# Kernel tuning notes

Measured on AMD Instinct MI355X. Metric: run time of the kernel, lower is better.

## Reference

```python
import jax, jax.numpy as jnp
import numpy as np

N = 65536
IN_DIM = 512
H1, H2 = 256, 128
LATENT = 3
SINDY_DIM = 22  # latent=3, poly_order=3: 3 ones + 3 linear + 6 quad + 10 cubic


def _mlp(v, w0, b0, w1, b1, w2, b2):
    # Linear+Sigmoid, Linear+Sigmoid, Linear+Identity (matches encoder/decoder stacks)
    h = jax.nn.sigmoid(v @ w0 + b0)
    h = jax.nn.sigmoid(h @ w1 + b1)
    return h @ w2 + b2


def _sindy_library(z):
    # Faithful to sindy_library(): d ones columns, then linear, quad (i<=j), cubic (i<=j<=k)
    n, d = z.shape
    cols = [jnp.ones((n,), z.dtype) for _ in range(d)]
    cols += [z[:, i] for i in range(d)]
    for i in range(d):
        for j in range(i, d):
            cols.append(z[:, i] * z[:, j])
    for i in range(d):
        for j in range(i, d):
            for k in range(j, d):
                cols.append(z[:, i] * z[:, j] * z[:, k])
    return jnp.stack(cols, axis=1)


def _mean_jac(fn, x):
    # torch: jacobian of batched fn, take block-diagonal (per-sample Jacobians), mean over samples
    return jax.vmap(jax.jacrev(fn))(x).mean(axis=0)


def setup_inputs():
    key = jax.random.key(0)
    ks = jax.random.split(key, 12)

    def glorot(k, i, o):
        return jax.random.normal(k, (i, o), jnp.float32) * np.float32(np.sqrt(2.0 / (i + o)))

    return {
        "x": jax.random.normal(ks[0], (N, IN_DIM), jnp.float32),
        "dx": jax.random.normal(ks[1], (N, IN_DIM), jnp.float32),
        "ddx": jax.random.normal(ks[2], (N, IN_DIM), jnp.float32),
        "enc_w0": glorot(ks[3], IN_DIM, H1), "enc_b0": jnp.zeros((H1,), jnp.float32),
        "enc_w1": glorot(ks[4], H1, H2), "enc_b1": jnp.zeros((H2,), jnp.float32),
        "enc_w2": glorot(ks[5], H2, LATENT), "enc_b2": jnp.zeros((LATENT,), jnp.float32),
        "dec_w0": glorot(ks[6], LATENT, H2), "dec_b0": jnp.zeros((H2,), jnp.float32),
        "dec_w1": glorot(ks[7], H2, H1), "dec_b1": jnp.zeros((H1,), jnp.float32),
        "dec_w2": glorot(ks[8], H1, IN_DIM), "dec_b2": jnp.zeros((IN_DIM,), jnp.float32),
        "E_w": jnp.ones((SINDY_DIM, LATENT), jnp.float32),  # nn.init.ones_ on E.weight
        "E_b": jnp.zeros((LATENT,), jnp.float32),
    }


def reference(x, dx, ddx, enc_w0, enc_b0, enc_w1, enc_b1, enc_w2, enc_b2,
              dec_w0, dec_b0, dec_w1, dec_b1, dec_w2, dec_b2, E_w, E_b):
    enc = lambda v: _mlp(v, enc_w0, enc_b0, enc_w1, enc_b1, enc_w2, enc_b2)
    dec = lambda v: _mlp(v, dec_w0, dec_b0, dec_w1, dec_b1, dec_w2, dec_b2)

    z = enc(x)                      # [N, LATENT]
    Je = _mean_jac(enc, x)          # [LATENT, IN_DIM]  batch-mean encoder Jacobian
    dz = dx @ Je.T                  # [N, LATENT]
    theta = _sindy_library(z)       # [N, SINDY_DIM]
    dzb = theta @ E_w + E_b         # [N, LATENT]  SINDy prediction E(theta)
    xb = dec(z)                     # [N, IN_DIM]
    Jd = _mean_jac(dec, z)          # [IN_DIM, LATENT]  batch-mean decoder Jacobian
    dxb = dzb @ Jd.T                # [N, IN_DIM]
    return (z, dz, dzb, xb, dxb)
```

## Files before the change

### kernel.cpp

```cpp
#include <hip/hip_runtime.h>

#define NROWS 65536

typedef unsigned short u16;
typedef short bf16x8 __attribute__((ext_vector_type(8)));
typedef u16 u16x8 __attribute__((ext_vector_type(8)));
typedef float f32x4 __attribute__((ext_vector_type(4)));

__device__ __forceinline__ u16 f2bf(float f) {
  unsigned int u = __builtin_bit_cast(unsigned int, f);
  u += 0x7FFFu + ((u >> 16) & 1u);
  return (u16)(u >> 16);
}
__device__ __forceinline__ float bf2f(u16 s) {
  return __builtin_bit_cast(float, (unsigned int)s << 16);
}

__global__ void prep_weights(const float* __restrict__ eW0, const float* __restrict__ eW1,
                             const float* __restrict__ dW1, const float* __restrict__ dW2,
                             u16* __restrict__ eW0t, u16* __restrict__ eW1t,
                             u16* __restrict__ dW1t, u16* __restrict__ dW2t) {
  const int idx = blockIdx.x * 256 + threadIdx.x;
  if (idx < 131072) {
    const int n = idx >> 9, k = idx & 511;
    eW0t[idx] = f2bf(eW0[k * 256 + n]);
  } else if (idx < 163840) {
    const int j = idx - 131072, n = j >> 8, k = j & 255;
    eW1t[j] = f2bf(eW1[k * 128 + n]);
  } else if (idx < 196608) {
    const int j = idx - 163840, n = j >> 7, k = j & 127;
    dW1t[j] = f2bf(dW1[k * 256 + n]);
  } else {
    const int j = idx - 196608, n = j >> 8, k = j & 255;
    dW2t[j] = f2bf(dW2[k * 512 + n]);
  }
}

template <int ACT, int A_F32>
__global__ __launch_bounds__(256, 2) void gemm_mfma(const void* __restrict__ Av,
                                                    const u16* __restrict__ Wt,
                                                    const float* __restrict__ bias,
                                                    void* __restrict__ Cv, int K, int Nc) {
  __shared__ u16 As[128 * 32];
  __shared__ u16 Bs[128 * 32];
  const int tid = threadIdx.x;
  const int lane = tid & 63;
  const int wave = tid >> 6;
  const int n0 = blockIdx.x * 128;
  const int m0 = blockIdx.y * 128;
  const int wm = (wave & 1) * 64;
  const int wn = (wave >> 1) * 64;
  const int q = lane >> 4;
  const int mr = lane & 15;

  f32x4 acc[4][4] = {};

  for (int k0 = 0; k0 < K; k0 += 32) {
    if (A_F32) {
      const float* A = (const float*)Av;
#pragma unroll
      for (int i = 0; i < 2; ++i) {
        const int c = tid + i * 256;
        const int r = c >> 2, p = c & 3;
        const int g = (p - (r >> 1)) & 3;
        const float* src = A + (size_t)(m0 + r) * K + k0 + g * 8;
        const float4 v0 = *(const float4*)src;
        const float4 v1 = *(const float4*)(src + 4);
        u16x8 w;
        w[0] = f2bf(v0.x); w[1] = f2bf(v0.y); w[2] = f2bf(v0.z); w[3] = f2bf(v0.w);
        w[4] = f2bf(v1.x); w[5] = f2bf(v1.y); w[6] = f2bf(v1.z); w[7] = f2bf(v1.w);
        *(u16x8*)&As[c * 8] = w;
      }
    } else {
      const u16* A = (const u16*)Av;
#pragma unroll
      for (int i = 0; i < 2; ++i) {
        const int c = tid + i * 256;
        const int r = c >> 2, p = c & 3;
        const int g = (p - (r >> 1)) & 3;
        __builtin_amdgcn_global_load_lds(
            (const __attribute__((address_space(1))) void*)(A + (size_t)(m0 + r) * K + k0 + g * 8),
            (__attribute__((address_space(3))) void*)&As[(i * 256 + wave * 64) * 8], 16, 0, 0);
      }
    }
    {
#pragma unroll
      for (int i = 0; i < 2; ++i) {
        const int c = tid + i * 256;
        const int r = c >> 2, p = c & 3;
        const int g = (p - (r >> 1)) & 3;
        __builtin_amdgcn_global_load_lds(
            (const __attribute__((address_space(1))) void*)(Wt + (size_t)(n0 + r) * K + k0 + g * 8),
            (__attribute__((address_space(3))) void*)&Bs[(i * 256 + wave * 64) * 8], 16, 0, 0);
      }
    }
    __syncthreads();

    bf16x8 af[4], bfr[4];
#pragma unroll
    for (int i = 0; i < 4; ++i) {
      const int r = wm + i * 16 + mr;
      const int col = (q + (r >> 1)) & 3;
      af[i] = *(const bf16x8*)&As[r * 32 + col * 8];
    }
#pragma unroll
    for (int j = 0; j < 4; ++j) {
      const int r = wn + j * 16 + mr;
      const int col = (q + (r >> 1)) & 3;
      bfr[j] = *(const bf16x8*)&Bs[r * 32 + col * 8];
    }
#pragma unroll
    for (int i = 0; i < 4; ++i)
#pragma unroll
      for (int j = 0; j < 4; ++j)
        acc[i][j] = __builtin_amdgcn_mfma_f32_16x16x32_bf16(af[i], bfr[j], acc[i][j], 0, 0, 0);
    __syncthreads();
  }

  const int orow = (lane >> 4) * 4;
  const int ocol = lane & 15;
#pragma unroll
  for (int j = 0; j < 4; ++j) {
    const int col = n0 + wn + j * 16 + ocol;
    const float bj = bias[col];
#pragma unroll
    for (int i = 0; i < 4; ++i) {
      const int rbase = m0 + wm + i * 16 + orow;
#pragma unroll
      for (int r = 0; r < 4; ++r) {
        float v = acc[i][j][r] + bj;
        if (ACT) {
          v = 1.0f / (1.0f + __expf(-v));
          ((u16*)Cv)[(size_t)(rbase + r) * Nc + col] = f2bf(v);
        } else {
          ((float*)Cv)[(size_t)(rbase + r) * Nc + col] = v;
        }
      }
    }
  }
}

__global__ void covar_bf16(const u16* __restrict__ P, const u16* __restrict__ Q,
                           float* __restrict__ partial, int Ap, int Bq, int chunk) {
  __shared__ float Ps[16][68];
  __shared__ float Qs[16][68];
  const int tid = threadIdx.x;
  const int a0 = blockIdx.x * 64;
  const int b0 = blockIdx.y * 64;
  const int nbase = blockIdx.z * chunk;
  const int tx = tid & 15, ty = tid >> 4;
  float acc[4][4] = {};
  for (int nn = 0; nn < chunk; nn += 16) {
    const int e = tid * 4;
    const int r = e >> 6;
    const int c = e & 63;
    {
      const ushort4 v = *(const ushort4*)(P + (size_t)(nbase + nn + r) * Ap + (a0 + c));
      const float p0 = bf2f(v.x), p1 = bf2f(v.y), p2 = bf2f(v.z), p3 = bf2f(v.w);
      Ps[r][c + 0] = p0 * (1.0f - p0);
      Ps[r][c + 1] = p1 * (1.0f - p1);
      Ps[r][c + 2] = p2 * (1.0f - p2);
      Ps[r][c + 3] = p3 * (1.0f - p3);
    }
    {
      const ushort4 u = *(const ushort4*)(Q + (size_t)(nbase + nn + r) * Bq + (b0 + c));
      const float q0 = bf2f(u.x), q1 = bf2f(u.y), q2 = bf2f(u.z), q3 = bf2f(u.w);
      Qs[r][c + 0] = q0 * (1.0f - q0);
      Qs[r][c + 1] = q1 * (1.0f - q1);
      Qs[r][c + 2] = q2 * (1.0f - q2);
      Qs[r][c + 3] = q3 * (1.0f - q3);
    }
    __syncthreads();
#pragma unroll
    for (int kk = 0; kk < 16; ++kk) {
      float a[4], b[4];
#pragma unroll
      for (int i = 0; i < 4; ++i) a[i] = Ps[kk][ty * 4 + i];
#pragma unroll
      for (int j = 0; j < 4; ++j) b[j] = Qs[kk][tx * 4 + j];
#pragma unroll
      for (int i = 0; i < 4; ++i)
#pragma unroll
        for (int j = 0; j < 4; ++j) acc[i][j] += a[i] * b[j];
    }
    __syncthreads();
  }
  float* out = partial + (size_t)blockIdx.z * Ap * Bq;
#pragma unroll
  for (int i = 0; i < 4; ++i)
#pragma unroll
    for (int j = 0; j < 4; ++j)
      out[(size_t)(a0 + ty * 4 + i) * Bq + (b0 + tx * 4 + j)] = acc[i][j];
}

__global__ void reduce_partial(const float* __restrict__ partial, float* __restrict__ out,
                               int S, int Z) {
  const int i = blockIdx.x * 256 + threadIdx.x;
  float s = 0.f;
  for (int z = 0; z < Z; ++z) s += partial[(size_t)z * S + i];
  out[i] = s;
}

__global__ void enc_l3_sindy(const u16* __restrict__ h2, const float* __restrict__ W2,
                             const float* __restrict__ b2, const float* __restrict__ Ew,
                             const float* __restrict__ Eb, float* __restrict__ z_out,
                             float* __restrict__ dzb_out) {
  const int lane = threadIdx.x & 63;
  const int row = blockIdx.x * 4 + (threadIdx.x >> 6);
  const ushort2 h = *(const ushort2*)(h2 + (size_t)row * 128 + lane * 2);
  const float hx = bf2f(h.x), hy = bf2f(h.y);
  const int k = lane * 2;
  float s[3];
#pragma unroll
  for (int l = 0; l < 3; ++l)
    s[l] = hx * W2[k * 3 + l] + hy * W2[(k + 1) * 3 + l];
#pragma unroll
  for (int off = 32; off > 0; off >>= 1) {
    s[0] += __shfl_xor(s[0], off);
    s[1] += __shfl_xor(s[1], off);
    s[2] += __shfl_xor(s[2], off);
  }
  if (lane == 0) {
    const float z0 = s[0] + b2[0];
    const float z1 = s[1] + b2[1];
    const float z2 = s[2] + b2[2];
    z_out[row * 3 + 0] = z0;
    z_out[row * 3 + 1] = z1;
    z_out[row * 3 + 2] = z2;
    float th[22];
    th[0] = 1.f; th[1] = 1.f; th[2] = 1.f;
    th[3] = z0; th[4] = z1; th[5] = z2;
    th[6] = z0 * z0; th[7] = z0 * z1; th[8] = z0 * z2;
    th[9] = z1 * z1; th[10] = z1 * z2; th[11] = z2 * z2;
    th[12] = z0 * z0 * z0; th[13] = z0 * z0 * z1; th[14] = z0 * z0 * z2;
    th[15] = z0 * z1 * z1; th[16] = z0 * z1 * z2; th[17] = z0 * z2 * z2;
    th[18] = z1 * z1 * z1; th[19] = z1 * z1 * z2; th[20] = z1 * z2 * z2;
    th[21] = z2 * z2 * z2;
    float d0 = Eb[0], d1 = Eb[1], d2 = Eb[2];
#pragma unroll
    for (int c = 0; c < 22; ++c) {
      d0 += th[c] * Ew[c * 3 + 0];
      d1 += th[c] * Ew[c * 3 + 1];
      d2 += th[c] * Ew[c * 3 + 2];
    }
    dzb_out[row * 3 + 0] = d0;
    dzb_out[row * 3 + 1] = d1;
    dzb_out[row * 3 + 2] = d2;
  }
}

__global__ void t1_kernel(const float* __restrict__ Ce, const float* __restrict__ W2,
                          const float* __restrict__ W1, float* __restrict__ T1) {
  const int l = blockIdx.x;
  const int b = threadIdx.x;
  float acc = 0.f;
  for (int a = 0; a < 128; ++a)
    acc += W2[a * 3 + l] * W1[b * 128 + a] * Ce[a * 256 + b];
  T1[l * 256 + b] = acc * (1.0f / 65536.0f);
}

__global__ void je_kernel(const float* __restrict__ T1, const float* __restrict__ W0,
                          float* __restrict__ Je) {
  const int k = blockIdx.x * 256 + threadIdx.x;
  const int l = blockIdx.y;
  float acc = 0.f;
  for (int b = 0; b < 256; ++b) acc += T1[l * 256 + b] * W0[(size_t)k * 256 + b];
  Je[l * 512 + k] = acc;
}

__global__ void t2_kernel(const float* __restrict__ Cd, const float* __restrict__ V1,
                          const float* __restrict__ V0, float* __restrict__ T2) {
  const int l = blockIdx.x;
  const int a = threadIdx.x;
  float acc = 0.f;
  for (int b = 0; b < 128; ++b)
    acc += Cd[a * 128 + b] * V1[b * 256 + a] * V0[l * 128 + b];
  T2[a * 3 + l] = acc * (1.0f / 65536.0f);
}

__global__ void jd_kernel(const float* __restrict__ T2, const float* __restrict__ V2,
                          float* __restrict__ Jd) {
  const int k = blockIdx.x * 256 + threadIdx.x;
  const int l = blockIdx.y;
  float acc = 0.f;
  for (int a = 0; a < 256; ++a) acc += V2[(size_t)a * 512 + k] * T2[a * 3 + l];
  Jd[k * 3 + l] = acc;
}

__global__ void dz_kernel(const float* __restrict__ dx, const float* __restrict__ Je,
                          float* __restrict__ dz) {
  __shared__ float sJe[1536];
  for (int i = threadIdx.x; i < 1536; i += 256) sJe[i] = Je[i];
  __syncthreads();
  const int lane = threadIdx.x & 63;
  const int row = blockIdx.x * 4 + (threadIdx.x >> 6);
  const int k = lane * 8;
  const float4 v0 = *(const float4*)(dx + (size_t)row * 512 + k);
  const float4 v1 = *(const float4*)(dx + (size_t)row * 512 + k + 4);
  float s[3];
#pragma unroll
  for (int l = 0; l < 3; ++l) {
    const float* j = sJe + l * 512 + k;
    s[l] = v0.x * j[0] + v0.y * j[1] + v0.z * j[2] + v0.w * j[3] +
           v1.x * j[4] + v1.y * j[5] + v1.z * j[6] + v1.w * j[7];
  }
#pragma unroll
  for (int off = 32; off > 0; off >>= 1) {
    s[0] += __shfl_xor(s[0], off);
    s[1] += __shfl_xor(s[1], off);
    s[2] += __shfl_xor(s[2], off);
  }
  if (lane == 0) {
    dz[row * 3 + 0] = s[0];
    dz[row * 3 + 1] = s[1];
    dz[row * 3 + 2] = s[2];
  }
}

__global__ void dec_l1(const float* __restrict__ z, const float* __restrict__ V0,
                       const float* __restrict__ b0, u16* __restrict__ h1d) {
  __shared__ float sW[512];
  for (int i = threadIdx.x; i < 512; i += 256)
    sW[i] = (i < 384) ? V0[i] : b0[i - 384];
  __syncthreads();
  const int idx = blockIdx.x * 256 + threadIdx.x;
  const int n = idx >> 7;
  const int j = idx & 127;
  const float z0 = z[n * 3 + 0], z1 = z[n * 3 + 1], z2 = z[n * 3 + 2];
  const float v = z0 * sW[j] + z1 * sW[128 + j] + z2 * sW[256 + j] + sW[384 + j];
  h1d[idx] = f2bf(1.0f / (1.0f + __expf(-v)));
}

__global__ void dxb_kernel(const float* __restrict__ dzb, const float* __restrict__ Jd,
                           float* __restrict__ dxb) {
  __shared__ float sJd[1536];
  for (int i = threadIdx.x; i < 1536; i += 256) sJd[i] = Jd[i];
  __syncthreads();
  const int idx = blockIdx.x * 256 + threadIdx.x;
  const int n = idx >> 9;
  const int k = idx & 511;
  const float d0 = dzb[n * 3 + 0], d1 = dzb[n * 3 + 1], d2 = dzb[n * 3 + 2];
  dxb[idx] = d0 * sJd[k * 3 + 0] + d1 * sJd[k * 3 + 1] + d2 * sJd[k * 3 + 2];
}

extern "C" void kernel_launch(void* const* d_in, const int* in_sizes, int n_in,
                              void* d_out, int out_size, void* d_ws, size_t ws_size,
                              hipStream_t stream) {
  const int N = NROWS;
  const float* x   = (const float*)d_in[0];
  const float* dx  = (const float*)d_in[1];
  const float* eW0 = (const float*)d_in[3];
  const float* eb0 = (const float*)d_in[4];
  const float* eW1 = (const float*)d_in[5];
  const float* eb1 = (const float*)d_in[6];
  const float* eW2 = (const float*)d_in[7];
  const float* eb2 = (const float*)d_in[8];
  const float* dW0 = (const float*)d_in[9];
  const float* db0 = (const float*)d_in[10];
  const float* dW1 = (const float*)d_in[11];
  const float* db1 = (const float*)d_in[12];
  const float* dW2 = (const float*)d_in[13];
  const float* db2 = (const float*)d_in[14];
  const float* Ew  = (const float*)d_in[15];
  const float* Eb  = (const float*)d_in[16];

  float* out = (float*)d_out;
  float* z_out   = out;
  float* dz_out  = out + (size_t)N * 3;
  float* dzb_out = out + (size_t)N * 6;
  float* xb_out  = out + (size_t)N * 9;
  float* dxb_out = out + (size_t)N * 9 + (size_t)N * 512;

  u16* h1e = (u16*)d_ws;
  u16* h2e = h1e + (size_t)N * 256;
  u16* h2d = h1e;
  u16* h1d = h2e;
  u16* wbuf = h2e + (size_t)N * 128;
  u16* eW0t = wbuf;
  u16* eW1t = eW0t + 131072;
  u16* dW1t = eW1t + 32768;
  u16* dW2t = dW1t + 32768;
  float* partial = (float*)(dW2t + 131072);
  float* Ce = partial + (size_t)128 * 32768;
  float* Cd = Ce + 32768;
  float* T1 = Cd + 32768;
  float* T2 = T1 + 768;
  float* Je = T2 + 768;
  float* Jd = Je + 1536;

  prep_weights<<<1280, 256, 0, stream>>>(eW0, eW1, dW1, dW2, eW0t, eW1t, dW1t, dW2t);

  gemm_mfma<1, 1><<<dim3(2, N / 128), 256, 0, stream>>>(x, eW0t, eb0, h1e, 512, 256);
  gemm_mfma<1, 0><<<dim3(1, N / 128), 256, 0, stream>>>(h1e, eW1t, eb1, h2e, 256, 128);
  enc_l3_sindy<<<N / 4, 256, 0, stream>>>(h2e, eW2, eb2, Ew, Eb, z_out, dzb_out);

  covar_bf16<<<dim3(2, 4, 128), 256, 0, stream>>>(h2e, h1e, partial, 128, 256, N / 128);
  reduce_partial<<<128, 256, 0, stream>>>(partial, Ce, 32768, 128);
  t1_kernel<<<3, 256, 0, stream>>>(Ce, eW2, eW1, T1);
  je_kernel<<<dim3(2, 3), 256, 0, stream>>>(T1, eW0, Je);
  dz_kernel<<<N / 4, 256, 0, stream>>>(dx, Je, dz_out);

  dec_l1<<<N * 128 / 256, 256, 0, stream>>>(z_out, dW0, db0, h1d);
  gemm_mfma<1, 0><<<dim3(2, N / 128), 256, 0, stream>>>(h1d, dW1t, db1, h2d, 128, 256);
  gemm_mfma<0, 0><<<dim3(4, N / 128), 256, 0, stream>>>(h2d, dW2t, db2, xb_out, 256, 512);

  covar_bf16<<<dim3(4, 2, 128), 256, 0, stream>>>(h2d, h1d, partial, 256, 128, N / 128);
  reduce_partial<<<128, 256, 0, stream>>>(partial, Cd, 32768, 128);
  t2_kernel<<<3, 256, 0, stream>>>(Cd, dW1, dW0, T2);
  jd_kernel<<<dim3(2, 3), 256, 0, stream>>>(T2, dW2, Jd);
  dxb_kernel<<<N * 512 / 256, 256, 0, stream>>>(dzb_out, Jd, dxb_out);
}
```

Measured before the change: 965.1 us.

## Enlarge covariance tiles, fuse Jacobian kernels, vectorize decoder-L1 and dxb kernels

The covariance kernel moves to 128x128 tiles with 8x8 register blocking per thread and vectorized LDS and global accesses, so it does more FMA work per shared-memory load. The T1/Je and T2/Jd kernel pairs are each merged into a single 768-thread block that keeps the intermediate in shared memory, removing two launches. dec_l1 and dxb now have each thread produce 8 contiguous outputs with vector stores and keep weights in registers instead of shared memory. In exchange, the covariance kernel runs fewer blocks with higher register pressure, and the fused Jacobian kernels run on a single block.

```diff
diff --git a/kernel.cpp b/kernel.cpp
--- a/kernel.cpp
+++ b/kernel.cpp
@@ -14,6 +14,10 @@
 }
 __device__ __forceinline__ float bf2f(u16 s) {
   return __builtin_bit_cast(float, (unsigned int)s << 16);
+}
+__device__ __forceinline__ float sigd(u16 s) {
+  const float p = bf2f(s);
+  return p * (1.0f - p);
 }
 
 __global__ void prep_weights(const float* __restrict__ eW0, const float* __restrict__ eW1,
@@ -140,57 +144,66 @@
   }
 }
 
-__global__ void covar_bf16(const u16* __restrict__ P, const u16* __restrict__ Q,
-                           float* __restrict__ partial, int Ap, int Bq, int chunk) {
-  __shared__ float Ps[16][68];
-  __shared__ float Qs[16][68];
+__global__ __launch_bounds__(256, 2) void covar128(const u16* __restrict__ P,
+                                                   const u16* __restrict__ Q,
+                                                   float* __restrict__ partial,
+                                                   int Ap, int Bq, int chunk) {
+  __shared__ float Ps[16][132];
+  __shared__ float Qs[16][132];
   const int tid = threadIdx.x;
-  const int a0 = blockIdx.x * 64;
-  const int b0 = blockIdx.y * 64;
+  const int a0 = blockIdx.x * 128;
+  const int b0 = blockIdx.y * 128;
   const int nbase = blockIdx.z * chunk;
   const int tx = tid & 15, ty = tid >> 4;
-  float acc[4][4] = {};
+  float acc[8][8] = {};
+
   for (int nn = 0; nn < chunk; nn += 16) {
-    const int e = tid * 4;
-    const int r = e >> 6;
-    const int c = e & 63;
     {
-      const ushort4 v = *(const ushort4*)(P + (size_t)(nbase + nn + r) * Ap + (a0 + c));
-      const float p0 = bf2f(v.x), p1 = bf2f(v.y), p2 = bf2f(v.z), p3 = bf2f(v.w);
-      Ps[r][c + 0] = p0 * (1.0f - p0);
-      Ps[r][c + 1] = p1 * (1.0f - p1);
-      Ps[r][c + 2] = p2 * (1.0f - p2);
-      Ps[r][c + 3] = p3 * (1.0f - p3);
+      const u16* pr = P + (size_t)(nbase + nn + ty) * Ap + a0;
+      const ushort4 v0 = *(const ushort4*)(pr + tx * 4);
+      const ushort4 v1 = *(const ushort4*)(pr + 64 + tx * 4);
+      float4 f0, f1;
+      f0.x = sigd(v0.x); f0.y = sigd(v0.y); f0.z = sigd(v0.z); f0.w = sigd(v0.w);
+      f1.x = sigd(v1.x); f1.y = sigd(v1.y); f1.z = sigd(v1.z); f1.w = sigd(v1.w);
+      *(float4*)&Ps[ty][tx * 4] = f0;
+      *(float4*)&Ps[ty][64 + tx * 4] = f1;
     }
     {
-      const ushort4 u = *(const ushort4*)(Q + (size_t)(nbase + nn + r) * Bq + (b0 + c));
-      const float q0 = bf2f(u.x), q1 = bf2f(u.y), q2 = bf2f(u.z), q3 = bf2f(u.w);
-      Qs[r][c + 0] = q0 * (1.0f - q0);
-      Qs[r][c + 1] = q1 * (1.0f - q1);
-      Qs[r][c + 2] = q2 * (1.0f - q2);
-      Qs[r][c + 3] = q3 * (1.0f - q3);
+      const u16* qr = Q + (size_t)(nbase + nn + ty) * Bq + b0;
+      const ushort4 v0 = *(const ushort4*)(qr + tx * 4);
+      const ushort4 v1 = *(const ushort4*)(qr + 64 + tx * 4);
+      float4 f0, f1;
+      f0.x = sigd(v0.x); f0.y = sigd(v0.y); f0.z = sigd(v0.z); f0.w = sigd(v0.w);
+      f1.x = sigd(v1.x); f1.y = sigd(v1.y); f1.z = sigd(v1.z); f1.w = sigd(v1.w);
+      *(float4*)&Qs[ty][tx * 4] = f0;
+      *(float4*)&Qs[ty][64 + tx * 4] = f1;
     }
     __syncthreads();
 #pragma unroll
     for (int kk = 0; kk < 16; ++kk) {
-      float a[4], b[4];
-#pragma unroll
-      for (int i = 0; i < 4; ++i) a[i] = Ps[kk][ty * 4 + i];
-#pragma unroll
-      for (int j = 0; j < 4; ++j) b[j] = Qs[kk][tx * 4 + j];
-#pragma unroll
-      for (int i = 0; i < 4; ++i)
-#pragma unroll
-        for (int j = 0; j < 4; ++j) acc[i][j] += a[i] * b[j];
+      float av[8], bv[8];
+      *(float4*)&av[0] = *(const float4*)&Ps[kk][ty * 4];
+      *(float4*)&av[4] = *(const float4*)&Ps[kk][64 + ty * 4];
+      *(float4*)&bv[0] = *(const float4*)&Qs[kk][tx * 4];
+      *(float4*)&bv[4] = *(const float4*)&Qs[kk][64 + tx * 4];
+#pragma unroll
+      for (int i = 0; i < 8; ++i)
+#pragma unroll
+        for (int j = 0; j < 8; ++j) acc[i][j] += av[i] * bv[j];
     }
     __syncthreads();
   }
-  float* out = partial + (size_t)blockIdx.z * Ap * Bq;
-#pragma unroll
-  for (int i = 0; i < 4; ++i)
-#pragma unroll
-    for (int j = 0; j < 4; ++j)
-      out[(size_t)(a0 + ty * 4 + i) * Bq + (b0 + tx * 4 + j)] = acc[i][j];
+
+  float* outp = partial + (size_t)blockIdx.z * Ap * Bq;
+#pragma unroll
+  for (int i = 0; i < 8; ++i) {
+    const int ar = (i < 4) ? (ty * 4 + i) : (64 + ty * 4 + (i - 4));
+    float4 v0, v1;
+    v0.x = acc[i][0]; v0.y = acc[i][1]; v0.z = acc[i][2]; v0.w = acc[i][3];
+    v1.x = acc[i][4]; v1.y = acc[i][5]; v1.z = acc[i][6]; v1.w = acc[i][7];
+    *(float4*)&outp[(size_t)(a0 + ar) * Bq + b0 + tx * 4] = v0;
+    *(float4*)&outp[(size_t)(a0 + ar) * Bq + b0 + 64 + tx * 4] = v1;
+  }
 }
 
 __global__ void reduce_partial(const float* __restrict__ partial, float* __restrict__ out,
@@ -249,42 +262,47 @@
   }
 }
 
-__global__ void t1_kernel(const float* __restrict__ Ce, const float* __restrict__ W2,
-                          const float* __restrict__ W1, float* __restrict__ T1) {
-  const int l = blockIdx.x;
-  const int b = threadIdx.x;
-  float acc = 0.f;
-  for (int a = 0; a < 128; ++a)
-    acc += W2[a * 3 + l] * W1[b * 128 + a] * Ce[a * 256 + b];
-  T1[l * 256 + b] = acc * (1.0f / 65536.0f);
-}
-
-__global__ void je_kernel(const float* __restrict__ T1, const float* __restrict__ W0,
-                          float* __restrict__ Je) {
-  const int k = blockIdx.x * 256 + threadIdx.x;
-  const int l = blockIdx.y;
-  float acc = 0.f;
-  for (int b = 0; b < 256; ++b) acc += T1[l * 256 + b] * W0[(size_t)k * 256 + b];
-  Je[l * 512 + k] = acc;
-}
-
-__global__ void t2_kernel(const float* __restrict__ Cd, const float* __restrict__ V1,
-                          const float* __restrict__ V0, float* __restrict__ T2) {
-  const int l = blockIdx.x;
-  const int a = threadIdx.x;
-  float acc = 0.f;
-  for (int b = 0; b < 128; ++b)
-    acc += Cd[a * 128 + b] * V1[b * 256 + a] * V0[l * 128 + b];
-  T2[a * 3 + l] = acc * (1.0f / 65536.0f);
-}
-
-__global__ void jd_kernel(const float* __restrict__ T2, const float* __restrict__ V2,
-                          float* __restrict__ Jd) {
-  const int k = blockIdx.x * 256 + threadIdx.x;
-  const int l = blockIdx.y;
-  float acc = 0.f;
-  for (int a = 0; a < 256; ++a) acc += V2[(size_t)a * 512 + k] * T2[a * 3 + l];
-  Jd[k * 3 + l] = acc;
+__global__ void t1je_kernel(const float* __restrict__ Ce, const float* __restrict__ W2,
+                            const float* __restrict__ W1, const float* __restrict__ W0,
+                            float* __restrict__ Je) {
+  __shared__ float T1s[768];
+  const int t = threadIdx.x;
+  {
+    const int b = t & 255, l = t >> 8;
+    float acc = 0.f;
+    for (int a = 0; a < 128; ++a)
+      acc += W2[a * 3 + l] * W1[b * 128 + a] * Ce[a * 256 + b];
+    T1s[l * 256 + b] = acc * (1.0f / 65536.0f);
+  }
+  __syncthreads();
+  for (int idx = t; idx < 1536; idx += 768) {
+    const int l = idx >> 9, k = idx & 511;
+    const float* t1r = &T1s[l * 256];
+    float acc = 0.f;
+    for (int b = 0; b < 256; ++b) acc += t1r[b] * W0[(size_t)k * 256 + b];
+    Je[l * 512 + k] = acc;
+  }
+}
+
+__global__ void t2jd_kernel(const float* __restrict__ Cd, const float* __restrict__ V1,
+                            const float* __restrict__ V0, const float* __restrict__ V2,
+                            float* __restrict__ Jd) {
+  __shared__ float T2s[768];
+  const int t = threadIdx.x;
+  {
+    const int a = t & 255, l = t >> 8;
+    float acc = 0.f;
+    for (int b = 0; b < 128; ++b)
+      acc += Cd[a * 128 + b] * V1[b * 256 + a] * V0[l * 128 + b];
+    T2s[a * 3 + l] = acc * (1.0f / 65536.0f);
+  }
+  __syncthreads();
+  for (int idx = t; idx < 1536; idx += 768) {
+    const int k = idx & 511, l = idx >> 9;
+    float acc = 0.f;
+    for (int a = 0; a < 256; ++a) acc += V2[(size_t)a * 512 + k] * T2s[a * 3 + l];
+    Jd[k * 3 + l] = acc;
+  }
 }
 
 __global__ void dz_kernel(const float* __restrict__ dx, const float* __restrict__ Je,
@@ -319,28 +337,49 @@
 
 __global__ void dec_l1(const float* __restrict__ z, const float* __restrict__ V0,
                        const float* __restrict__ b0, u16* __restrict__ h1d) {
-  __shared__ float sW[512];
-  for (int i = threadIdx.x; i < 512; i += 256)
-    sW[i] = (i < 384) ? V0[i] : b0[i - 384];
-  __syncthreads();
-  const int idx = blockIdx.x * 256 + threadIdx.x;
-  const int n = idx >> 7;
-  const int j = idx & 127;
+  const int t = threadIdx.x;
+  const int j0 = (t & 15) * 8;
+  const int n = blockIdx.x * 16 + (t >> 4);
+  float w0[8], w1[8], w2[8], bb[8];
+  *(float4*)&w0[0] = *(const float4*)(V0 + j0);
+  *(float4*)&w0[4] = *(const float4*)(V0 + j0 + 4);
+  *(float4*)&w1[0] = *(const float4*)(V0 + 128 + j0);
+  *(float4*)&w1[4] = *(const float4*)(V0 + 128 + j0 + 4);
+  *(float4*)&w2[0] = *(const float4*)(V0 + 256 + j0);
+  *(float4*)&w2[4] = *(const float4*)(V0 + 256 + j0 + 4);
+  *(float4*)&bb[0] = *(const float4*)(b0 + j0);
+  *(float4*)&bb[4] = *(const float4*)(b0 + j0 + 4);
   const float z0 = z[n * 3 + 0], z1 = z[n * 3 + 1], z2 = z[n * 3 + 2];
-  const float v = z0 * sW[j] + z1 * sW[128 + j] + z2 * sW[256 + j] + sW[384 + j];
-  h1d[idx] = f2bf(1.0f / (1.0f + __expf(-v)));
+  u16x8 o;
+#pragma unroll
+  for (int m = 0; m < 8; ++m) {
+    const float v = z0 * w0[m] + z1 * w1[m] + z2 * w2[m] + bb[m];
+    o[m] = f2bf(1.0f / (1.0f + __expf(-v)));
+  }
+  *(u16x8*)(h1d + (size_t)n * 128 + j0) = o;
 }
 
 __global__ void dxb_kernel(const float* __restrict__ dzb, const float* __restrict__ Jd,
                            float* __restrict__ dxb) {
-  __shared__ float sJd[1536];
-  for (int i = threadIdx.x; i < 1536; i += 256) sJd[i] = Jd[i];
-  __syncthreads();
-  const int idx = blockIdx.x * 256 + threadIdx.x;
-  const int n = idx >> 9;
-  const int k = idx & 511;
-  const float d0 = dzb[n * 3 + 0], d1 = dzb[n * 3 + 1], d2 = dzb[n * 3 + 2];
-  dxb[idx] = d0 * sJd[k * 3 + 0] + d1 * sJd[k * 3 + 1] + d2 * sJd[k * 3 + 2];
+  const int t = threadIdx.x;
+  const int k0 = (t & 63) * 8;
+  const int rbase = blockIdx.x * 16 + (t >> 6);
+  float jf[24];
+#pragma unroll
+  for (int q = 0; q < 6; ++q)
+    *(float4*)&jf[q * 4] = *(const float4*)(Jd + k0 * 3 + q * 4);
+#pragma unroll
+  for (int it = 0; it < 4; ++it) {
+    const int n = rbase + it * 4;
+    const float d0 = dzb[n * 3 + 0], d1 = dzb[n * 3 + 1], d2 = dzb[n * 3 + 2];
+    float v[8];
+#pragma unroll
+    for (int m = 0; m < 8; ++m)
+      v[m] = d0 * jf[m * 3 + 0] + d1 * jf[m * 3 + 1] + d2 * jf[m * 3 + 2];
+    float* outp = dxb + (size_t)n * 512 + k0;
+    *(float4*)&outp[0] = *(float4*)&v[0];
+    *(float4*)&outp[4] = *(float4*)&v[4];
+  }
 }
 
 extern "C" void kernel_launch(void* const* d_in, const int* in_sizes, int n_in,
@@ -383,9 +422,7 @@
   float* partial = (float*)(dW2t + 131072);
   float* Ce = partial + (size_t)128 * 32768;
   float* Cd = Ce + 32768;
-  float* T1 = Cd + 32768;
-  float* T2 = T1 + 768;
-  float* Je = T2 + 768;
+  float* Je = Cd + 32768;
   float* Jd = Je + 1536;
 
   prep_weights<<<1280, 256, 0, stream>>>(eW0, eW1, dW1, dW2, eW0t, eW1t, dW1t, dW2t);
@@ -394,19 +431,17 @@
   gemm_mfma<1, 0><<<dim3(1, N / 128), 256, 0, stream>>>(h1e, eW1t, eb1, h2e, 256, 128);
   enc_l3_sindy<<<N / 4, 256, 0, stream>>>(h2e, eW2, eb2, Ew, Eb, z_out, dzb_out);
 
-  covar_bf16<<<dim3(2, 4, 128), 256, 0, stream>>>(h2e, h1e, partial, 128, 256, N / 128);
+  covar128<<<dim3(1, 2, 128), 256, 0, stream>>>(h2e, h1e, partial, 128, 256, N / 128);
   reduce_partial<<<128, 256, 0, stream>>>(partial, Ce, 32768, 128);
-  t1_kernel<<<3, 256, 0, stream>>>(Ce, eW2, eW1, T1);
-  je_kernel<<<dim3(2, 3), 256, 0, stream>>>(T1, eW0, Je);
+  t1je_kernel<<<1, 768, 0, stream>>>(Ce, eW2, eW1, eW0, Je);
   dz_kernel<<<N / 4, 256, 0, stream>>>(dx, Je, dz_out);
 
-  dec_l1<<<N * 128 / 256, 256, 0, stream>>>(z_out, dW0, db0, h1d);
+  dec_l1<<<N / 16, 256, 0, stream>>>(z_out, dW0, db0, h1d);
   gemm_mfma<1, 0><<<dim3(2, N / 128), 256, 0, stream>>>(h1d, dW1t, db1, h2d, 128, 256);
   gemm_mfma<0, 0><<<dim3(4, N / 128), 256, 0, stream>>>(h2d, dW2t, db2, xb_out, 256, 512);
 
-  covar_bf16<<<dim3(4, 2, 128), 256, 0, stream>>>(h2d, h1d, partial, 256, 128, N / 128);
+  covar128<<<dim3(2, 1, 128), 256, 0, stream>>>(h2d, h1d, partial, 256, 128, N / 128);
   reduce_partial<<<128, 256, 0, stream>>>(partial, Cd, 32768, 128);
-  t2_kernel<<<3, 256, 0, stream>>>(Cd, dW1, dW0, T2);
-  jd_kernel<<<dim3(2, 3), 256, 0, stream>>>(T2, dW2, Jd);
-  dxb_kernel<<<N * 512 / 256, 256, 0, stream>>>(dzb_out, Jd, dxb_out);
-}
+  t2jd_kernel<<<1, 768, 0, stream>>>(Cd, dW1, dW0, dW2, Jd);
+  dxb_kernel<<<N / 16, 256, 0, stream>>>(dzb_out, Jd, dxb_out);
+}
```

New measurement: 960.6 us. No clear change (-0.5%).
